# Performance work log

Measured on AMD Instinct MI355X. Metric: run time of the kernel, lower is better.

The kernel has to match this reference:

```python
import jax, jax.numpy as jnp
import numpy as np

N = 100000
E = 3200000
N_IN = 512
N_OUT = 256


def setup_inputs() -> dict:
    key = jax.random.key(0)
    k = jax.random.split(key, 6)
    stdv = 1.0 / np.sqrt(N_IN)
    x = jax.random.normal(k[0], (N, N_IN), dtype=jnp.float32)
    adj_rows = jax.random.randint(k[1], (E,), 0, N, dtype=jnp.int32)
    adj_cols = jax.random.randint(k[2], (E,), 0, N, dtype=jnp.int32)
    adj_vals = jax.random.uniform(k[3], (E,), dtype=jnp.float32)
    W = jax.random.uniform(k[4], (N_OUT, N_IN), minval=-stdv, maxval=stdv, dtype=jnp.float32)
    b = jax.random.uniform(k[5], (N_OUT,), minval=-stdv, maxval=stdv, dtype=jnp.float32)
    return {"x": x, "adj_rows": adj_rows, "adj_cols": adj_cols, "adj_vals": adj_vals, "W": W, "b": b}


def reference(x, adj_rows, adj_cols, adj_vals, W, b):
    # linear projection: x @ W^T + b  -> [N, n_out]
    h = jnp.einsum('ni,oi->no', x, W) + b
    # spmm: out[r] = sum_e adj_vals[e] * h[adj_cols[e]] for edges with row r
    msgs = h[adj_cols] * adj_vals[:, None]          # [E, n_out]
    out = jax.ops.segment_sum(msgs, adj_rows, num_segments=N)
    return out
```

## Files before the change

kernel.cpp:

```cpp
#include <hip/hip_runtime.h>

#define NIN 512
#define NOUT 256
#define NPART 8
#define RPB 32
#define BSH 5
#define CHUNK 2048
#define CSH 11
#define SEG 256
#define SEGSH 8
#define SCAT 2048

typedef __attribute__((ext_vector_type(8))) __bf16 bf16x8;
typedef __attribute__((ext_vector_type(4))) float f32x4;
typedef __attribute__((ext_vector_type(8))) float f32x8;
typedef __attribute__((ext_vector_type(2))) int i32x2;
typedef __attribute__((ext_vector_type(8))) ushort u16x8;

__device__ __forceinline__ ushort f2bf(float f) {
  return __builtin_bit_cast(ushort, (__bf16)f);
}
__device__ __forceinline__ uint pk2(float a, float b) {
  return (uint)f2bf(a) | ((uint)f2bf(b) << 16);
}
__device__ __forceinline__ float bf2f(ushort u) {
  return __builtin_bit_cast(float, (uint)u << 16);
}

__global__ __launch_bounds__(256) void init_cur_kernel(int* __restrict__ cur,
                                                       int NB) {
  int i = blockIdx.x * 256 + threadIdx.x;
  if (i < NPART * NB) {
    int s = i / NB;
    int b = i - s * NB;
    cur[i] = ((b << 3) + s) << SEGSH;
  }
}

__global__ __launch_bounds__(512) void gemm_scatter_kernel(
    const float* __restrict__ x, const float* __restrict__ W,
    const float* __restrict__ bias, ushort* __restrict__ h, int M,
    const int* __restrict__ rows, const int* __restrict__ cols,
    const float* __restrict__ vals, int* __restrict__ cur,
    int2* __restrict__ bufE, int E, int NB, int nchunks, int G) {
  __shared__ ushort a_lds[128 * 40];
  __shared__ ushort b_lds[256 * 40];

  const int t = threadIdx.x;

  if (blockIdx.x >= G) {
    const int s = blockIdx.x & (NPART - 1);
    const int j = (int)blockIdx.x - G;
    const int m = j >> 3;
    const int nres = SCAT >> 3;
    int* mycur = cur + s * NB;
    for (int k = m;; k += nres) {
      int c = k * NPART + s;
      if (c >= nchunks) break;
      int i0 = c << CSH;
      int i1 = min(E, i0 + CHUNK);
      for (int i = i0 + t; i < i1; i += 1024) {
        int ib = i + 512;
        bool hb = ib < i1;
        int r0 = __builtin_nontemporal_load(&rows[i]);
        int c0 = __builtin_nontemporal_load(&cols[i]);
        float v0 = __builtin_nontemporal_load(&vals[i]);
        int r1 = 0, c1 = 0;
        float v1 = 0.f;
        if (hb) {
          r1 = __builtin_nontemporal_load(&rows[ib]);
          c1 = __builtin_nontemporal_load(&cols[ib]);
          v1 = __builtin_nontemporal_load(&vals[ib]);
        }
        int pos0 = atomicAdd(&mycur[r0 >> BSH], 1);
        int pos1 = hb ? atomicAdd(&mycur[r1 >> BSH], 1) : 0;
        int2 p0;
        p0.x = ((r0 & (RPB - 1)) << 17) | c0;
        p0.y = __builtin_bit_cast(int, v0);
        bufE[pos0] = p0;
        if (hb) {
          int2 p1;
          p1.x = ((r1 & (RPB - 1)) << 17) | c1;
          p1.y = __builtin_bit_cast(int, v1);
          bufE[pos1] = p1;
        }
      }
    }
    return;
  }

  const int l = t & 63;
  const int wv = t >> 6;
  const int wr = wv >> 2;
  const int wc = wv & 3;
  const int m0 = blockIdx.x * 128;

  const int lrow = l & 15;
  const int lk = (l >> 4) * 8;

  f32x4 acc[4][4];
#pragma unroll
  for (int i = 0; i < 4; ++i)
#pragma unroll
    for (int j = 0; j < 4; ++j) acc[i][j] = (f32x4){0.f, 0.f, 0.f, 0.f};

  float biasr[4];
#pragma unroll
  for (int j = 0; j < 4; ++j) biasr[j] = bias[wc * 64 + j * 16 + lrow];

  const int arow = t >> 2;
  const int akc = (t & 3) * 8;
  const int brow = t >> 1;
  const int bkc = (t & 1) * 16;

  const bool avalid = (m0 + arow < M);
  const float* xbase = x + (size_t)(m0 + arow) * NIN + akc;
  const float* wbase = W + (size_t)brow * NIN + bkc;

  float4 xa = make_float4(0.f, 0.f, 0.f, 0.f), xb = xa;
  if (avalid) {
    const float4* xs = reinterpret_cast<const float4*>(xbase);
    xa = xs[0];
    xb = xs[1];
  }
  float4 w0, w1, w2, w3;
  {
    const float4* ws = reinterpret_cast<const float4*>(wbase);
    w0 = ws[0]; w1 = ws[1]; w2 = ws[2]; w3 = ws[3];
  }

  for (int kk = 0; kk < 16; ++kk) {
    const int k0 = kk * 32;
    {
      uint4 p;
      p.x = pk2(xa.x, xa.y); p.y = pk2(xa.z, xa.w);
      p.z = pk2(xb.x, xb.y); p.w = pk2(xb.z, xb.w);
      *reinterpret_cast<uint4*>(&a_lds[arow * 40 + akc]) = p;
    }
    {
      uint4 p0, p1;
      p0.x = pk2(w0.x, w0.y); p0.y = pk2(w0.z, w0.w);
      p0.z = pk2(w1.x, w1.y); p0.w = pk2(w1.z, w1.w);
      p1.x = pk2(w2.x, w2.y); p1.y = pk2(w2.z, w2.w);
      p1.z = pk2(w3.x, w3.y); p1.w = pk2(w3.z, w3.w);
      *reinterpret_cast<uint4*>(&b_lds[brow * 40 + bkc]) = p0;
      *reinterpret_cast<uint4*>(&b_lds[brow * 40 + bkc + 8]) = p1;
    }
    __syncthreads();

    if (kk < 15) {
      if (avalid) {
        const float4* xs = reinterpret_cast<const float4*>(xbase + k0 + 32);
        xa = xs[0];
        xb = xs[1];
      }
      const float4* ws = reinterpret_cast<const float4*>(wbase + k0 + 32);
      w0 = ws[0]; w1 = ws[1]; w2 = ws[2]; w3 = ws[3];
    }

    bf16x8 af[4], bf_[4];
#pragma unroll
    for (int i = 0; i < 4; ++i)
      af[i] = *reinterpret_cast<const bf16x8*>(
          &a_lds[(wr * 64 + i * 16 + lrow) * 40 + lk]);
#pragma unroll
    for (int j = 0; j < 4; ++j)
      bf_[j] = *reinterpret_cast<const bf16x8*>(
          &b_lds[(wc * 64 + j * 16 + lrow) * 40 + lk]);
#pragma unroll
    for (int i = 0; i < 4; ++i)
#pragma unroll
      for (int j = 0; j < 4; ++j)
        acc[i][j] = __builtin_amdgcn_mfma_f32_16x16x32_bf16(af[i], bf_[j],
                                                            acc[i][j], 0, 0, 0);
    __syncthreads();
  }

#pragma unroll
  for (int i = 0; i < 4; ++i) {
    const int mbase = m0 + wr * 64 + i * 16 + (l >> 4) * 4;
#pragma unroll
    for (int r = 0; r < 4; ++r) {
      int m = mbase + r;
      if (m >= M) continue;
#pragma unroll
      for (int j = 0; j < 4; ++j)
        h[(size_t)m * NOUT + wc * 64 + j * 16 + lrow] =
            f2bf(acc[i][j][r] + biasr[j]);
    }
  }
}

__global__ __launch_bounds__(256) void bucket_reduce_kernel(
    const ushort* __restrict__ h, const int2* __restrict__ bufE,
    const int* __restrict__ cur, float* __restrict__ out, int M, int NB) {
  __shared__ int2 sbuf[NPART * SEG];
  __shared__ int cnt[RPB];
  __shared__ int off[RPB + 1];
  __shared__ int segn[NPART];

  const int b = blockIdx.x;
  const int t = threadIdx.x;

  if (t < NPART)
    segn[t] = min(cur[t * NB + b] - (((b << 3) + t) << SEGSH), SEG);
  if (t < RPB) cnt[t] = 0;
  __syncthreads();

  int2 ed[NPART];
#pragma unroll
  for (int s = 0; s < NPART; ++s) {
    int2 p = make_int2(0, 0);
    if (t < segn[s]) {
      i32x2 raw = __builtin_nontemporal_load(reinterpret_cast<const i32x2*>(
          &bufE[(size_t)(((b << 3) + s) << SEGSH) + t]));
      p.x = raw.x;
      p.y = raw.y;
      atomicAdd(&cnt[(uint)p.x >> 17], 1);
    }
    ed[s] = p;
  }
  __syncthreads();
  if (t == 0) {
    int run = 0;
#pragma unroll
    for (int j = 0; j < RPB; ++j) { off[j] = run; run += cnt[j]; }
    off[RPB] = run;
  }
  __syncthreads();
  if (t < RPB) cnt[t] = off[t];
  __syncthreads();
#pragma unroll
  for (int s = 0; s < NPART; ++s) {
    if (t < segn[s]) {
      int pos = atomicAdd(&cnt[(uint)ed[s].x >> 17], 1);
      sbuf[pos] = ed[s];
    }
  }
  __syncthreads();

  const int wv = t >> 6;
  const int lane = t & 63;
  const int half = lane >> 5;
  const int hl = lane & 31;
  for (int q = 0; q < 8; ++q) {
    int j = wv * 8 + q;
    int row = b * RPB + j;
    if (row >= M) break;
    int e = off[j];
    const int e1 = off[j + 1];
    f32x8 acc = (f32x8){0.f, 0.f, 0.f, 0.f, 0.f, 0.f, 0.f, 0.f};
    for (; e + 15 < e1; e += 16) {
      u16x8 hv[8];
      float vv[8];
#pragma unroll
      for (int u = 0; u < 8; ++u) {
        int2 p = sbuf[e + 2 * u + half];
        vv[u] = __builtin_bit_cast(float, p.y);
        hv[u] = *reinterpret_cast<const u16x8*>(
            h + (size_t)(p.x & 0x1FFFF) * NOUT + hl * 8);
      }
#pragma unroll
      for (int u = 0; u < 8; ++u)
#pragma unroll
        for (int c = 0; c < 8; ++c) acc[c] += vv[u] * bf2f(hv[u][c]);
    }
    for (; e + 7 < e1; e += 8) {
      u16x8 hv[4];
      float vv[4];
#pragma unroll
      for (int u = 0; u < 4; ++u) {
        int2 p = sbuf[e + 2 * u + half];
        vv[u] = __builtin_bit_cast(float, p.y);
        hv[u] = *reinterpret_cast<const u16x8*>(
            h + (size_t)(p.x & 0x1FFFF) * NOUT + hl * 8);
      }
#pragma unroll
      for (int u = 0; u < 4; ++u)
#pragma unroll
        for (int c = 0; c < 8; ++c) acc[c] += vv[u] * bf2f(hv[u][c]);
    }
    for (; e + 1 < e1; e += 2) {
      int2 p = sbuf[e + half];
      float v = __builtin_bit_cast(float, p.y);
      u16x8 hv = *reinterpret_cast<const u16x8*>(
          h + (size_t)(p.x & 0x1FFFF) * NOUT + hl * 8);
#pragma unroll
      for (int c = 0; c < 8; ++c) acc[c] += v * bf2f(hv[c]);
    }
    if (e < e1) {
      int2 p = sbuf[e];
      float v = half ? 0.f : __builtin_bit_cast(float, p.y);
      u16x8 hv = *reinterpret_cast<const u16x8*>(
          h + (size_t)(p.x & 0x1FFFF) * NOUT + hl * 8);
#pragma unroll
      for (int c = 0; c < 8; ++c) acc[c] += v * bf2f(hv[c]);
    }
#pragma unroll
    for (int c = 0; c < 8; ++c) acc[c] += __shfl(acc[c], hl + 32);
    if (half == 0) {
      f32x4 lo = (f32x4){acc[0], acc[1], acc[2], acc[3]};
      f32x4 hi = (f32x4){acc[4], acc[5], acc[6], acc[7]};
      f32x4* dst = reinterpret_cast<f32x4*>(out + (size_t)row * NOUT + hl * 8);
      __builtin_nontemporal_store(lo, dst);
      __builtin_nontemporal_store(hi, dst + 1);
    }
  }
}

extern "C" void kernel_launch(void* const* d_in, const int* in_sizes, int n_in,
                              void* d_out, int out_size, void* d_ws, size_t ws_size,
                              hipStream_t stream) {
  const float* x        = (const float*)d_in[0];
  const int*   adj_rows = (const int*)d_in[1];
  const int*   adj_cols = (const int*)d_in[2];
  const float* adj_vals = (const float*)d_in[3];
  const float* W        = (const float*)d_in[4];
  const float* b        = (const float*)d_in[5];
  float* out = (float*)d_out;

  const int M = in_sizes[0] / NIN;
  const int E = in_sizes[1];

  const int NB = (M + RPB - 1) >> BSH;
  const int nchunks = (E + CHUNK - 1) >> CSH;

  ushort* h    = (ushort*)d_ws;
  int2*   bufE = (int2*)(h + (size_t)M * NOUT);
  int*    cur  = (int*)(bufE + (size_t)NB * NPART * SEG);

  const int G = (M + 127) / 128;

  init_cur_kernel<<<(NPART * NB + 255) / 256, 256, 0, stream>>>(cur, NB);
  gemm_scatter_kernel<<<G + SCAT, 512, 0, stream>>>(
      x, W, b, h, M, adj_rows, adj_cols, adj_vals, cur, bufE, E, NB, nchunks, G);
  bucket_reduce_kernel<<<NB, 256, 0, stream>>>(h, bufE, cur, out, M, NB);
}
```

Measured before the change: 423.9 us.

## Load GEMM tiles directly into LDS as fp32 via global_load_lds, convert on read

Replaces the register-staged, prefetched global loads with bf16 packing into padded LDS by direct global-to-LDS 16-byte async loads that keep fp32 tiles in unpadded LDS. Conversion to bf16 now happens after reading from LDS, right before the MFMAs. This cuts register pressure and VALU packing work on the store side. In exchange it drops the software prefetch overlap, doubles LDS footprint and read traffic, likely adds bank conflicts from unpadded 32-float rows, and redoes the conversion in every wave that reads a tile.

```diff
diff --git a/kernel.cpp b/kernel.cpp
--- a/kernel.cpp
+++ b/kernel.cpp
@@ -17,11 +17,13 @@
 typedef __attribute__((ext_vector_type(2))) int i32x2;
 typedef __attribute__((ext_vector_type(8))) ushort u16x8;
 
+#define GLOAD16(gp, lp)                                                   \
+  __builtin_amdgcn_global_load_lds(                                       \
+      (const __attribute__((address_space(1))) unsigned int*)(gp),        \
+      (__attribute__((address_space(3))) unsigned int*)(lp), 16, 0, 0)
+
 __device__ __forceinline__ ushort f2bf(float f) {
   return __builtin_bit_cast(ushort, (__bf16)f);
-}
-__device__ __forceinline__ uint pk2(float a, float b) {
-  return (uint)f2bf(a) | ((uint)f2bf(b) << 16);
 }
 __device__ __forceinline__ float bf2f(ushort u) {
   return __builtin_bit_cast(float, (uint)u << 16);
@@ -43,8 +45,8 @@
     const int* __restrict__ rows, const int* __restrict__ cols,
     const float* __restrict__ vals, int* __restrict__ cur,
     int2* __restrict__ bufE, int E, int NB, int nchunks, int G) {
-  __shared__ ushort a_lds[128 * 40];
-  __shared__ ushort b_lds[256 * 40];
+  __shared__ float a_lds[128 * 32];
+  __shared__ float b_lds[256 * 32];
 
   const int t = threadIdx.x;
 
@@ -96,7 +98,9 @@
   const int m0 = blockIdx.x * 128;
 
   const int lrow = l & 15;
-  const int lk = (l >> 4) * 8;
+  const int lk8 = (l >> 4) * 8;
+  const int lr8 = l >> 3;
+  const int lc4 = (l & 7) * 4;
 
   f32x4 acc[4][4];
 #pragma unroll
@@ -107,66 +111,49 @@
   float biasr[4];
 #pragma unroll
   for (int j = 0; j < 4; ++j) biasr[j] = bias[wc * 64 + j * 16 + lrow];
-
-  const int arow = t >> 2;
-  const int akc = (t & 3) * 8;
-  const int brow = t >> 1;
-  const int bkc = (t & 1) * 16;
-
-  const bool avalid = (m0 + arow < M);
-  const float* xbase = x + (size_t)(m0 + arow) * NIN + akc;
-  const float* wbase = W + (size_t)brow * NIN + bkc;
-
-  float4 xa = make_float4(0.f, 0.f, 0.f, 0.f), xb = xa;
-  if (avalid) {
-    const float4* xs = reinterpret_cast<const float4*>(xbase);
-    xa = xs[0];
-    xb = xs[1];
-  }
-  float4 w0, w1, w2, w3;
-  {
-    const float4* ws = reinterpret_cast<const float4*>(wbase);
-    w0 = ws[0]; w1 = ws[1]; w2 = ws[2]; w3 = ws[3];
-  }
 
   for (int kk = 0; kk < 16; ++kk) {
     const int k0 = kk * 32;
-    {
-      uint4 p;
-      p.x = pk2(xa.x, xa.y); p.y = pk2(xa.z, xa.w);
-      p.z = pk2(xb.x, xb.y); p.w = pk2(xb.z, xb.w);
-      *reinterpret_cast<uint4*>(&a_lds[arow * 40 + akc]) = p;
-    }
-    {
-      uint4 p0, p1;
-      p0.x = pk2(w0.x, w0.y); p0.y = pk2(w0.z, w0.w);
-      p0.z = pk2(w1.x, w1.y); p0.w = pk2(w1.z, w1.w);
-      p1.x = pk2(w2.x, w2.y); p1.y = pk2(w2.z, w2.w);
-      p1.z = pk2(w3.x, w3.y); p1.w = pk2(w3.z, w3.w);
-      *reinterpret_cast<uint4*>(&b_lds[brow * 40 + bkc]) = p0;
-      *reinterpret_cast<uint4*>(&b_lds[brow * 40 + bkc + 8]) = p1;
+#pragma unroll
+    for (int q = 0; q < 2; ++q) {
+      const int r0 = (wv * 2 + q) * 8;
+      const int gr = min(m0 + r0 + lr8, M - 1);
+      const float* gp = x + (size_t)gr * NIN + k0 + lc4;
+      GLOAD16(gp, a_lds + r0 * 32);
+    }
+#pragma unroll
+    for (int q = 0; q < 4; ++q) {
+      const int n0 = (wv * 4 + q) * 8;
+      const float* gp = W + (size_t)(n0 + lr8) * NIN + k0 + lc4;
+      GLOAD16(gp, b_lds + n0 * 32);
     }
     __syncthreads();
 
-    if (kk < 15) {
-      if (avalid) {
-        const float4* xs = reinterpret_cast<const float4*>(xbase + k0 + 32);
-        xa = xs[0];
-        xb = xs[1];
-      }
-      const float4* ws = reinterpret_cast<const float4*>(wbase + k0 + 32);
-      w0 = ws[0]; w1 = ws[1]; w2 = ws[2]; w3 = ws[3];
-    }
-
     bf16x8 af[4], bf_[4];
 #pragma unroll
-    for (int i = 0; i < 4; ++i)
-      af[i] = *reinterpret_cast<const bf16x8*>(
-          &a_lds[(wr * 64 + i * 16 + lrow) * 40 + lk]);
-#pragma unroll
-    for (int j = 0; j < 4; ++j)
-      bf_[j] = *reinterpret_cast<const bf16x8*>(
-          &b_lds[(wc * 64 + j * 16 + lrow) * 40 + lk]);
+    for (int i = 0; i < 4; ++i) {
+      const float* p = a_lds + (wr * 64 + i * 16 + lrow) * 32 + lk8;
+      f32x4 lo = *reinterpret_cast<const f32x4*>(p);
+      f32x4 hi = *reinterpret_cast<const f32x4*>(p + 4);
+      bf16x8 v;
+      v[0] = (__bf16)lo[0]; v[1] = (__bf16)lo[1];
+      v[2] = (__bf16)lo[2]; v[3] = (__bf16)lo[3];
+      v[4] = (__bf16)hi[0]; v[5] = (__bf16)hi[1];
+      v[6] = (__bf16)hi[2]; v[7] = (__bf16)hi[3];
+      af[i] = v;
+    }
+#pragma unroll
+    for (int j = 0; j < 4; ++j) {
+      const float* p = b_lds + (wc * 64 + j * 16 + lrow) * 32 + lk8;
+      f32x4 lo = *reinterpret_cast<const f32x4*>(p);
+      f32x4 hi = *reinterpret_cast<const f32x4*>(p + 4);
+      bf16x8 v;
+      v[0] = (__bf16)lo[0]; v[1] = (__bf16)lo[1];
+      v[2] = (__bf16)lo[2]; v[3] = (__bf16)lo[3];
+      v[4] = (__bf16)hi[0]; v[5] = (__bf16)hi[1];
+      v[6] = (__bf16)hi[2]; v[7] = (__bf16)hi[3];
+      bf_[j] = v;
+    }
 #pragma unroll
     for (int i = 0; i < 4; ++i)
 #pragma unroll
```

Result: no change. 428.7 us (+1.1%).
